# Kernel optimization log

Hardware: AMD Instinct MI355X
Metric: run time of the kernel (lower is better)

## Reference

```python
import jax, jax.numpy as jnp
import numpy as np

N_NODES = 100000
N_EDGES = 1600000
VOCAB = 1000
EMB_DIM = 64
OUT_DIM = 32


def setup_inputs() -> dict:
    key = jax.random.key(0)
    k1, k2, k3, k4, k5 = jax.random.split(key, 5)
    node_seq = jax.random.randint(k1, (N_NODES,), 0, VOCAB, dtype=jnp.int64)
    edge_index = jax.random.randint(k2, (2, N_EDGES), 0, N_NODES, dtype=jnp.int64)
    edge_weight = jax.random.uniform(k3, (N_EDGES,), dtype=jnp.float32)
    emb = jax.random.normal(k4, (VOCAB, EMB_DIM), dtype=jnp.float32)
    W = jax.random.normal(k5, (EMB_DIM, OUT_DIM), dtype=jnp.float32) * (1.0 / np.sqrt(EMB_DIM))
    b = jnp.zeros((OUT_DIM,), dtype=jnp.float32)
    return {"node_seq": node_seq, "edge_index": edge_index, "edge_weight": edge_weight,
            "emb": emb, "W": W, "b": b}


def reference(node_seq, edge_index, edge_weight, emb, W, b):
    N = node_seq.shape[0]
    # Embedding lookup: [N, EMB_DIM]
    x = emb[node_seq]
    # Linear transform first (GCNConv applies lin before propagate): [N, OUT_DIM]
    xw = x @ W
    # Add self loops with weight 1 (PyG GCNConv default add_self_loops=True, fill_value=1)
    loop = jnp.arange(N, dtype=edge_index.dtype)
    row = jnp.concatenate([edge_index[0], loop])
    col = jnp.concatenate([edge_index[1], loop])
    w = jnp.concatenate([edge_weight, jnp.ones((N,), dtype=edge_weight.dtype)])
    # Symmetric gcn_norm: deg over targets, norm = d^{-1/2}[row] * w * d^{-1/2}[col]
    deg = jax.ops.segment_sum(w, col, num_segments=N)
    dis = jnp.where(deg > 0, jax.lax.rsqrt(jnp.where(deg > 0, deg, 1.0)), 0.0)
    norm = dis[row] * w * dis[col]
    # Gather messages from source nodes, scale, scatter-add into targets
    msgs = norm[:, None] * xw[row]            # [E+N, OUT_DIM]
    out = jax.ops.segment_sum(msgs, col, num_segments=N) + b  # [N, OUT_DIM]
    # Mean pool over nodes
    return out.mean(axis=0)
```

## Files before the change

kernel.cpp:

```cpp
#include <hip/hip_runtime.h>

#define N_NODES 100000
#define N_EDGES 1600000
#define VOCAB   1000
#define EMB_DIM 64
#define OUT_DIM 32

#define BKT_BITS 9
#define BKT_SIZE 512
#define NBKT ((N_NODES + BKT_SIZE - 1) / BKT_SIZE)
#define CAP  12288
#define NSB  512
#define CHUNK (N_EDGES / NSB)

#define NBC 256
#define TBC 512

__device__ __forceinline__ void fatomic_add(float* p, float v) {
    unsafeAtomicAdd(p, v);
}

__global__ void k_init(int* __restrict__ cursors) {
    int i = blockIdx.x * blockDim.x + threadIdx.x;
    if (i < NBKT) cursors[i] = i * CAP;
}

__global__ void __launch_bounds__(256) k_scatter(
        const int* __restrict__ row, const int* __restrict__ col,
        const float* __restrict__ w, int* __restrict__ cursors,
        uint2* __restrict__ recs) {
    __shared__ uint2 stage[CHUNK];
    __shared__ unsigned char seg[CHUNK];
    __shared__ int cnt[NBKT], lofs[NBKT], gbase[NBKT];
    __shared__ int sc[256];
    const int tid = threadIdx.x;
    const int e0 = blockIdx.x * CHUNK;

    for (int i = tid; i < NBKT; i += 256) cnt[i] = 0;
    __syncthreads();
    for (int i = tid; i < CHUNK; i += 256)
        atomicAdd(&cnt[col[e0 + i] >> BKT_BITS], 1);
    __syncthreads();
    sc[tid] = (tid < NBKT) ? cnt[tid] : 0;
    __syncthreads();
    for (int d = 1; d < 256; d <<= 1) {
        int v = (tid >= d) ? sc[tid - d] : 0;
        __syncthreads();
        sc[tid] += v;
        __syncthreads();
    }
    if (tid < NBKT) {
        lofs[tid]  = sc[tid] - cnt[tid];
        gbase[tid] = atomicAdd(&cursors[tid], cnt[tid]);
        cnt[tid]   = 0;
    }
    __syncthreads();
    for (int i = tid; i < CHUNK; i += 256) {
        int c = col[e0 + i];
        int r = row[e0 + i];
        int b = c >> BKT_BITS;
        int p = lofs[b] + atomicAdd(&cnt[b], 1);
        stage[p] = make_uint2(((unsigned)r << BKT_BITS) | (unsigned)(c & (BKT_SIZE - 1)),
                              __float_as_uint(w[e0 + i]));
        seg[p] = (unsigned char)b;
    }
    __syncthreads();
    for (int i = tid; i < CHUNK; i += 256) {
        int b = seg[i];
        recs[gbase[b] + (i - lofs[b])] = stage[i];
    }
}

__global__ void __launch_bounds__(256) k_dis(
        const uint2* __restrict__ recs, const int* __restrict__ cursors,
        const int* __restrict__ node_seq, uint2* __restrict__ disseq) {
    __shared__ float acc[BKT_SIZE];
    const int b = blockIdx.x;
    for (int i = threadIdx.x; i < BKT_SIZE; i += 256) acc[i] = 0.0f;
    __syncthreads();
    const int base = b * CAP;
    const int cnt = cursors[b] - base;
    for (int i = threadIdx.x; i < cnt; i += 256) {
        uint2 r = recs[base + i];
        fatomic_add(&acc[r.x & (BKT_SIZE - 1)], __uint_as_float(r.y));
    }
    __syncthreads();
    const int n0 = b << BKT_BITS;
    for (int i = threadIdx.x; i < BKT_SIZE && n0 + i < N_NODES; i += 256)
        disseq[n0 + i] = make_uint2(__float_as_uint(__frsqrt_rn(1.0f + acc[i])),
                                    (unsigned)node_seq[n0 + i]);
}

__global__ void __launch_bounds__(512) k_coeff(
        const uint2* __restrict__ recs, const int* __restrict__ cursors,
        const uint2* __restrict__ disseq, float* __restrict__ gcoeff) {
    __shared__ float dloc[BKT_SIZE];
    __shared__ float lc[VOCAB];
    const int b = blockIdx.x;
    const int n0 = b << BKT_BITS;
    for (int i = threadIdx.x; i < VOCAB; i += 512) lc[i] = 0.0f;
    if (threadIdx.x < BKT_SIZE) {
        int n = n0 + threadIdx.x;
        dloc[threadIdx.x] = (n < N_NODES) ? __uint_as_float(disseq[n].x) : 0.0f;
    }
    __syncthreads();
    const int base = b * CAP;
    const int cnt = cursors[b] - base;
    for (int i = threadIdx.x; i < cnt; i += 512) {
        uint2 rec = recs[base + i];
        int lcol = rec.x & (BKT_SIZE - 1);
        int r    = rec.x >> BKT_BITS;
        uint2 ds = disseq[r];
        float norm = __uint_as_float(ds.x) * __uint_as_float(rec.y) * dloc[lcol];
        fatomic_add(&lc[ds.y], norm);
    }
    if (threadIdx.x < BKT_SIZE) {
        int n = n0 + threadIdx.x;
        if (n < N_NODES) {
            uint2 ds = disseq[n];
            float d = __uint_as_float(ds.x);
            fatomic_add(&lc[ds.y], d * d);
        }
    }
    __syncthreads();
    for (int i = threadIdx.x; i < VOCAB; i += 512)
        gcoeff[b * VOCAB + i] = lc[i];
}

__global__ void k_init_deg(float* __restrict__ deg) {
    int i = blockIdx.x * blockDim.x + threadIdx.x;
    if (i < N_NODES) deg[i] = 1.0f;
}
__global__ void k_deg(const int* __restrict__ col, const float* __restrict__ w,
                      float* __restrict__ deg) {
    int i = blockIdx.x * blockDim.x + threadIdx.x;
    if (i < N_EDGES) fatomic_add(&deg[col[i]], w[i]);
}
__global__ void k_dis_fb(float* __restrict__ deg) {
    int i = blockIdx.x * blockDim.x + threadIdx.x;
    if (i < N_NODES) deg[i] = __frsqrt_rn(deg[i]);
}
__global__ void __launch_bounds__(TBC) k_coeff_stream(
        const int* __restrict__ row, const int* __restrict__ col,
        const float* __restrict__ w, const float* __restrict__ dis,
        const int* __restrict__ node_seq, float* __restrict__ gcoeff) {
    __shared__ float lc[VOCAB];
    for (int i = threadIdx.x; i < VOCAB; i += TBC) lc[i] = 0.0f;
    __syncthreads();
    const int total = N_EDGES + N_NODES;
    const int stride = NBC * TBC;
    for (int i = blockIdx.x * TBC + threadIdx.x; i < total; i += stride) {
        if (i < N_EDGES) {
            int r = row[i];
            fatomic_add(&lc[node_seq[r]], dis[r] * w[i] * dis[col[i]]);
        } else {
            int n = i - N_EDGES;
            float d = dis[n];
            fatomic_add(&lc[node_seq[n]], d * d);
        }
    }
    __syncthreads();
    for (int i = threadIdx.x; i < VOCAB; i += TBC)
        gcoeff[blockIdx.x * VOCAB + i] = lc[i];
}

__global__ void __launch_bounds__(256) k_reduce(
        const float* __restrict__ gcoeff, float* __restrict__ coeff, int npart) {
    int g = blockIdx.x * 256 + threadIdx.x;
    int v = g >> 6;
    int l = g & 63;
    if (v >= VOCAB) return;
    float s = 0.0f;
    for (int p = l; p < npart; p += 64) s += gcoeff[p * VOCAB + v];
    for (int off = 32; off > 0; off >>= 1) s += __shfl_down(s, off, 64);
    if (l == 0) coeff[v] = s;
}

__global__ void __launch_bounds__(1024) k_final(
        const float* __restrict__ coeff, const float* __restrict__ emb,
        const float* __restrict__ W, const float* __restrict__ bias,
        float* __restrict__ out) {
    __shared__ float lc[VOCAB];
    __shared__ float tk[16 * 64];
    int t = threadIdx.x;
    for (int v = t; v < VOCAB; v += 1024) lc[v] = coeff[v];
    __syncthreads();

    int k = t & 63;
    int g = t >> 6;
    float p = 0.0f;
    for (int v = g; v < VOCAB; v += 16) p += lc[v] * emb[v * EMB_DIM + k];
    tk[g * 64 + k] = p;
    __syncthreads();

    if (t < 64) {
        float s = 0.0f;
        for (int gg = 0; gg < 16; ++gg) s += tk[gg * 64 + t];
        tk[t] = s;
    }
    __syncthreads();

    if (t < OUT_DIM) {
        float s = 0.0f;
        for (int kk = 0; kk < EMB_DIM; ++kk) s += tk[kk] * W[kk * OUT_DIM + t];
        out[t] = s * (1.0f / (float)N_NODES) + bias[t];
    }
}

extern "C" void kernel_launch(void* const* d_in, const int* in_sizes, int n_in,
                              void* d_out, int out_size, void* d_ws, size_t ws_size,
                              hipStream_t stream) {
    const int*   node_seq = (const int*)  d_in[0];
    const int*   eidx     = (const int*)  d_in[1];
    const float* ew       = (const float*)d_in[2];
    const float* emb      = (const float*)d_in[3];
    const float* W        = (const float*)d_in[4];
    const float* b        = (const float*)d_in[5];
    float*       out      = (float*)d_out;

    const int* row = eidx;
    const int* col = eidx + N_EDGES;

    char* wsb = (char*)d_ws;
    const size_t REC_BYTES = (size_t)NBKT * CAP * sizeof(uint2);
    const size_t need = REC_BYTES + 4096 + (size_t)N_NODES * 8
                      + (size_t)NBKT * VOCAB * 4 + VOCAB * 4 + 4096;

    if (ws_size >= need) {
        uint2* recs    = (uint2*)wsb;
        int*   cursors = (int*)(wsb + REC_BYTES);
        uint2* disseq  = (uint2*)(wsb + REC_BYTES + 4096);
        float* gcoeff  = (float*)(disseq + N_NODES);
        float* coeff   = gcoeff + (size_t)NBKT * VOCAB;

        k_init<<<1, 256, 0, stream>>>(cursors);
        k_scatter<<<NSB, 256, 0, stream>>>(row, col, ew, cursors, recs);
        k_dis<<<NBKT, 256, 0, stream>>>(recs, cursors, node_seq, disseq);
        k_coeff<<<NBKT, 512, 0, stream>>>(recs, cursors, disseq, gcoeff);
        k_reduce<<<(VOCAB * 64 + 255) / 256, 256, 0, stream>>>(gcoeff, coeff, NBKT);
        k_final<<<1, 1024, 0, stream>>>(coeff, emb, W, b, out);
    } else {
        float* dis    = (float*)wsb;
        float* gcoeff = dis + N_NODES;
        float* coeff  = gcoeff + (size_t)NBC * VOCAB;

        k_init_deg<<<(N_NODES + 255) / 256, 256, 0, stream>>>(dis);
        k_deg<<<(N_EDGES + 255) / 256, 256, 0, stream>>>(col, ew, dis);
        k_dis_fb<<<(N_NODES + 255) / 256, 256, 0, stream>>>(dis);
        k_coeff_stream<<<NBC, TBC, 0, stream>>>(row, col, ew, dis, node_seq, gcoeff);
        k_reduce<<<(VOCAB * 64 + 255) / 256, 256, 0, stream>>>(gcoeff, coeff, NBC);
        k_final<<<1, 1024, 0, stream>>>(coeff, emb, W, b, out);
    }
}
```

Before: 145.6 us.

## Fuse GCN pipeline into one cooperative kernel with grid syncs

Replaces the chain of six kernel launches with a single cooperative kernel that runs the phases (cursor init, bucket scatter, degree/dis, coefficient accumulation, reduction, final projection) separated by grid.sync(). The goal is to remove per-launch overhead and idle gaps between small kernels. The coefficient phase also splits each bucket across two blocks for more parallelism. The risks are grid-sync cost, lower occupancy from the large shared footprint (about 17KB plus other arrays at 512 threads), and the cooperative launch failing, which falls back to the old path. The fallback path also drops the workspace-size check and reduces gcoeff over NBKT partitions, while coeff is now placed after NPART partitions.

Result: slower. 423.0 us (+190.5%).

```diff
diff --git a/kernel.cpp b/kernel.cpp
--- a/kernel.cpp
+++ b/kernel.cpp
@@ -1,4 +1,7 @@
 #include <hip/hip_runtime.h>
+#include <hip/hip_cooperative_groups.h>
+
+namespace cg = cooperative_groups;
 
 #define N_NODES 100000
 #define N_EDGES 1600000
@@ -10,35 +13,193 @@
 #define BKT_SIZE 512
 #define NBKT ((N_NODES + BKT_SIZE - 1) / BKT_SIZE)
 #define CAP  12288
-#define NSB  512
-#define CHUNK (N_EDGES / NSB)
-
-#define NBC 256
-#define TBC 512
+#define GRID 512
+#define TPB  512
+#define CHUNK (N_EDGES / GRID)
+#define SPLIT 2
+#define NPART (NBKT * SPLIT)
 
 __device__ __forceinline__ void fatomic_add(float* p, float v) {
     unsafeAtomicAdd(p, v);
+}
+
+__global__ void __launch_bounds__(TPB, 4) k_fused(
+        const int* __restrict__ node_seq, const int* __restrict__ row,
+        const int* __restrict__ col, const float* __restrict__ ew,
+        const float* __restrict__ emb, const float* __restrict__ W,
+        const float* __restrict__ bias, float* __restrict__ out,
+        int* __restrict__ cursors, uint2* __restrict__ recs,
+        uint2* __restrict__ disseq, float* __restrict__ gcoeff,
+        float* __restrict__ coeff)
+{
+    cg::grid_group grid = cg::this_grid();
+    __shared__ uint2 stage[CHUNK];
+    __shared__ unsigned char seg[CHUNK];
+    __shared__ int cnt[NBKT], lofs[NBKT], gbase[NBKT];
+    __shared__ int sc[TPB];
+    __shared__ float acc[BKT_SIZE];
+    __shared__ float lc[VOCAB];
+    __shared__ float tk[8 * 64];
+
+    const int tid = threadIdx.x;
+    const int bid = blockIdx.x;
+
+    {
+        int g = bid * TPB + tid;
+        if (g < NBKT) cursors[g] = g * CAP;
+    }
+    grid.sync();
+
+    {
+        const int e0 = bid * CHUNK;
+        for (int i = tid; i < NBKT; i += TPB) cnt[i] = 0;
+        __syncthreads();
+        for (int i = tid; i < CHUNK; i += TPB)
+            atomicAdd(&cnt[col[e0 + i] >> BKT_BITS], 1);
+        __syncthreads();
+        sc[tid] = (tid < NBKT) ? cnt[tid] : 0;
+        __syncthreads();
+        for (int d = 1; d < TPB; d <<= 1) {
+            int v = (tid >= d) ? sc[tid - d] : 0;
+            __syncthreads();
+            sc[tid] += v;
+            __syncthreads();
+        }
+        if (tid < NBKT) {
+            lofs[tid]  = sc[tid] - cnt[tid];
+            gbase[tid] = atomicAdd(&cursors[tid], cnt[tid]);
+            cnt[tid]   = 0;
+        }
+        __syncthreads();
+        for (int i = tid; i < CHUNK; i += TPB) {
+            int c = col[e0 + i];
+            int r = row[e0 + i];
+            int b = c >> BKT_BITS;
+            int p = lofs[b] + atomicAdd(&cnt[b], 1);
+            stage[p] = make_uint2(((unsigned)r << BKT_BITS) | (unsigned)(c & (BKT_SIZE - 1)),
+                                  __float_as_uint(ew[e0 + i]));
+            seg[p] = (unsigned char)b;
+        }
+        __syncthreads();
+        for (int i = tid; i < CHUNK; i += TPB) {
+            int b = seg[i];
+            recs[gbase[b] + (i - lofs[b])] = stage[i];
+        }
+    }
+    grid.sync();
+
+    if (bid < NBKT) {
+        const int b = bid;
+        for (int i = tid; i < BKT_SIZE; i += TPB) acc[i] = 0.0f;
+        __syncthreads();
+        const int base = b * CAP;
+        const int c2 = cursors[b] - base;
+        for (int i = tid; i < c2; i += TPB) {
+            uint2 rr = recs[base + i];
+            fatomic_add(&acc[rr.x & (BKT_SIZE - 1)], __uint_as_float(rr.y));
+        }
+        __syncthreads();
+        const int n0 = b << BKT_BITS;
+        for (int i = tid; i < BKT_SIZE; i += TPB) {
+            int n = n0 + i;
+            if (n < N_NODES)
+                disseq[n] = make_uint2(__float_as_uint(__frsqrt_rn(1.0f + acc[i])),
+                                       (unsigned)node_seq[n]);
+        }
+    }
+    grid.sync();
+
+    if (bid < NPART) {
+        const int b = bid >> 1, half = bid & 1;
+        const int n0 = b << BKT_BITS;
+        for (int i = tid; i < VOCAB; i += TPB) lc[i] = 0.0f;
+        if (tid < BKT_SIZE) {
+            int n = n0 + tid;
+            acc[tid] = (n < N_NODES) ? __uint_as_float(disseq[n].x) : 0.0f;
+        }
+        __syncthreads();
+        const int base = b * CAP;
+        const int c3 = cursors[b] - base;
+        const int lo = half ? (c3 + 1) / 2 : 0;
+        const int hi = half ? c3 : (c3 + 1) / 2;
+        for (int i = lo + tid; i < hi; i += TPB) {
+            uint2 rec = recs[base + i];
+            int lcol = rec.x & (BKT_SIZE - 1);
+            int r    = rec.x >> BKT_BITS;
+            uint2 ds = disseq[r];
+            fatomic_add(&lc[ds.y],
+                __uint_as_float(ds.x) * __uint_as_float(rec.y) * acc[lcol]);
+        }
+        if (half == 0 && tid < BKT_SIZE) {
+            int n = n0 + tid;
+            if (n < N_NODES) {
+                uint2 ds = disseq[n];
+                float d = __uint_as_float(ds.x);
+                fatomic_add(&lc[ds.y], d * d);
+            }
+        }
+        __syncthreads();
+        for (int i = tid; i < VOCAB; i += TPB)
+            gcoeff[bid * VOCAB + i] = lc[i];
+    }
+    grid.sync();
+
+    {
+        int gw = (bid * TPB + tid) >> 6;
+        int l  = tid & 63;
+        if (gw < VOCAB) {
+            float s = 0.0f;
+            for (int p = l; p < NPART; p += 64) s += gcoeff[p * VOCAB + gw];
+            for (int off = 32; off > 0; off >>= 1) s += __shfl_down(s, off, 64);
+            if (l == 0) coeff[gw] = s;
+        }
+    }
+    grid.sync();
+
+    if (bid == 0) {
+        for (int v = tid; v < VOCAB; v += TPB) lc[v] = coeff[v];
+        __syncthreads();
+        int k = tid & 63;
+        int g = tid >> 6;
+        float p = 0.0f;
+        for (int v = g; v < VOCAB; v += 8) p += lc[v] * emb[v * EMB_DIM + k];
+        tk[g * 64 + k] = p;
+        __syncthreads();
+        if (tid < 64) {
+            float s = 0.0f;
+            for (int gg = 0; gg < 8; ++gg) s += tk[gg * 64 + tid];
+            tk[tid] = s;
+        }
+        __syncthreads();
+        if (tid < OUT_DIM) {
+            float s = 0.0f;
+            for (int kk = 0; kk < EMB_DIM; ++kk) s += tk[kk] * W[kk * OUT_DIM + tid];
+            out[tid] = s * (1.0f / (float)N_NODES) + bias[tid];
+        }
+    }
 }
 
 __global__ void k_init(int* __restrict__ cursors) {
     int i = blockIdx.x * blockDim.x + threadIdx.x;
     if (i < NBKT) cursors[i] = i * CAP;
 }
+
+#define NSB  512
+#define FCHUNK (N_EDGES / NSB)
 
 __global__ void __launch_bounds__(256) k_scatter(
         const int* __restrict__ row, const int* __restrict__ col,
         const float* __restrict__ w, int* __restrict__ cursors,
         uint2* __restrict__ recs) {
-    __shared__ uint2 stage[CHUNK];
-    __shared__ unsigned char seg[CHUNK];
+    __shared__ uint2 stage[FCHUNK];
+    __shared__ unsigned char seg[FCHUNK];
     __shared__ int cnt[NBKT], lofs[NBKT], gbase[NBKT];
     __shared__ int sc[256];
     const int tid = threadIdx.x;
-    const int e0 = blockIdx.x * CHUNK;
-
+    const int e0 = blockIdx.x * FCHUNK;
     for (int i = tid; i < NBKT; i += 256) cnt[i] = 0;
     __syncthreads();
-    for (int i = tid; i < CHUNK; i += 256)
+    for (int i = tid; i < FCHUNK; i += 256)
         atomicAdd(&cnt[col[e0 + i] >> BKT_BITS], 1);
     __syncthreads();
     sc[tid] = (tid < NBKT) ? cnt[tid] : 0;
@@ -55,7 +216,7 @@
         cnt[tid]   = 0;
     }
     __syncthreads();
-    for (int i = tid; i < CHUNK; i += 256) {
+    for (int i = tid; i < FCHUNK; i += 256) {
         int c = col[e0 + i];
         int r = row[e0 + i];
         int b = c >> BKT_BITS;
@@ -65,7 +226,7 @@
         seg[p] = (unsigned char)b;
     }
     __syncthreads();
-    for (int i = tid; i < CHUNK; i += 256) {
+    for (int i = tid; i < FCHUNK; i += 256) {
         int b = seg[i];
         recs[gbase[b] + (i - lofs[b])] = stage[i];
     }
@@ -111,8 +272,8 @@
         int lcol = rec.x & (BKT_SIZE - 1);
         int r    = rec.x >> BKT_BITS;
         uint2 ds = disseq[r];
-        float norm = __uint_as_float(ds.x) * __uint_as_float(rec.y) * dloc[lcol];
-        fatomic_add(&lc[ds.y], norm);
+        fatomic_add(&lc[ds.y],
+            __uint_as_float(ds.x) * __uint_as_float(rec.y) * dloc[lcol]);
     }
     if (threadIdx.x < BKT_SIZE) {
         int n = n0 + threadIdx.x;
@@ -125,43 +286,6 @@
     __syncthreads();
     for (int i = threadIdx.x; i < VOCAB; i += 512)
         gcoeff[b * VOCAB + i] = lc[i];
-}
-
-__global__ void k_init_deg(float* __restrict__ deg) {
-    int i = blockIdx.x * blockDim.x + threadIdx.x;
-    if (i < N_NODES) deg[i] = 1.0f;
-}
-__global__ void k_deg(const int* __restrict__ col, const float* __restrict__ w,
-                      float* __restrict__ deg) {
-    int i = blockIdx.x * blockDim.x + threadIdx.x;
-    if (i < N_EDGES) fatomic_add(&deg[col[i]], w[i]);
-}
-__global__ void k_dis_fb(float* __restrict__ deg) {
-    int i = blockIdx.x * blockDim.x + threadIdx.x;
-    if (i < N_NODES) deg[i] = __frsqrt_rn(deg[i]);
-}
-__global__ void __launch_bounds__(TBC) k_coeff_stream(
-        const int* __restrict__ row, const int* __restrict__ col,
-        const float* __restrict__ w, const float* __restrict__ dis,
-        const int* __restrict__ node_seq, float* __restrict__ gcoeff) {
-    __shared__ float lc[VOCAB];
-    for (int i = threadIdx.x; i < VOCAB; i += TBC) lc[i] = 0.0f;
-    __syncthreads();
-    const int total = N_EDGES + N_NODES;
-    const int stride = NBC * TBC;
-    for (int i = blockIdx.x * TBC + threadIdx.x; i < total; i += stride) {
-        if (i < N_EDGES) {
-            int r = row[i];
-            fatomic_add(&lc[node_seq[r]], dis[r] * w[i] * dis[col[i]]);
-        } else {
-            int n = i - N_EDGES;
-            float d = dis[n];
-            fatomic_add(&lc[node_seq[n]], d * d);
-        }
-    }
-    __syncthreads();
-    for (int i = threadIdx.x; i < VOCAB; i += TBC)
-        gcoeff[blockIdx.x * VOCAB + i] = lc[i];
 }
 
 __global__ void __launch_bounds__(256) k_reduce(
@@ -185,21 +309,18 @@
     int t = threadIdx.x;
     for (int v = t; v < VOCAB; v += 1024) lc[v] = coeff[v];
     __syncthreads();
-
     int k = t & 63;
     int g = t >> 6;
     float p = 0.0f;
     for (int v = g; v < VOCAB; v += 16) p += lc[v] * emb[v * EMB_DIM + k];
     tk[g * 64 + k] = p;
     __syncthreads();
-
     if (t < 64) {
         float s = 0.0f;
         for (int gg = 0; gg < 16; ++gg) s += tk[gg * 64 + t];
         tk[t] = s;
     }
     __syncthreads();
-
     if (t < OUT_DIM) {
         float s = 0.0f;
         for (int kk = 0; kk < EMB_DIM; ++kk) s += tk[kk] * W[kk * OUT_DIM + t];
@@ -215,7 +336,7 @@
     const float* ew       = (const float*)d_in[2];
     const float* emb      = (const float*)d_in[3];
     const float* W        = (const float*)d_in[4];
-    const float* b        = (const float*)d_in[5];
+    const float* bias     = (const float*)d_in[5];
     float*       out      = (float*)d_out;
 
     const int* row = eidx;
@@ -223,32 +344,25 @@
 
     char* wsb = (char*)d_ws;
     const size_t REC_BYTES = (size_t)NBKT * CAP * sizeof(uint2);
-    const size_t need = REC_BYTES + 4096 + (size_t)N_NODES * 8
-                      + (size_t)NBKT * VOCAB * 4 + VOCAB * 4 + 4096;
-
-    if (ws_size >= need) {
-        uint2* recs    = (uint2*)wsb;
-        int*   cursors = (int*)(wsb + REC_BYTES);
-        uint2* disseq  = (uint2*)(wsb + REC_BYTES + 4096);
-        float* gcoeff  = (float*)(disseq + N_NODES);
-        float* coeff   = gcoeff + (size_t)NBKT * VOCAB;
-
+    uint2* recs    = (uint2*)wsb;
+    int*   cursors = (int*)(wsb + REC_BYTES);
+    uint2* disseq  = (uint2*)(wsb + REC_BYTES + 4096);
+    float* gcoeff  = (float*)(disseq + N_NODES);
+    float* coeff   = gcoeff + (size_t)NPART * VOCAB;
+
+    void* args[] = {(void*)&node_seq, (void*)&row, (void*)&col, (void*)&ew,
+                    (void*)&emb, (void*)&W, (void*)&bias, (void*)&out,
+                    (void*)&cursors, (void*)&recs, (void*)&disseq,
+                    (void*)&gcoeff, (void*)&coeff};
+    hipError_t err = hipLaunchCooperativeKernel((const void*)k_fused,
+                                                dim3(GRID), dim3(TPB),
+                                                args, 0, stream);
+    if (err != hipSuccess) {
         k_init<<<1, 256, 0, stream>>>(cursors);
         k_scatter<<<NSB, 256, 0, stream>>>(row, col, ew, cursors, recs);
         k_dis<<<NBKT, 256, 0, stream>>>(recs, cursors, node_seq, disseq);
         k_coeff<<<NBKT, 512, 0, stream>>>(recs, cursors, disseq, gcoeff);
         k_reduce<<<(VOCAB * 64 + 255) / 256, 256, 0, stream>>>(gcoeff, coeff, NBKT);
-        k_final<<<1, 1024, 0, stream>>>(coeff, emb, W, b, out);
-    } else {
-        float* dis    = (float*)wsb;
-        float* gcoeff = dis + N_NODES;
-        float* coeff  = gcoeff + (size_t)NBC * VOCAB;
-
-        k_init_deg<<<(N_NODES + 255) / 256, 256, 0, stream>>>(dis);
-        k_deg<<<(N_EDGES + 255) / 256, 256, 0, stream>>>(col, ew, dis);
-        k_dis_fb<<<(N_NODES + 255) / 256, 256, 0, stream>>>(dis);
-        k_coeff_stream<<<NBC, TBC, 0, stream>>>(row, col, ew, dis, node_seq, gcoeff);
-        k_reduce<<<(VOCAB * 64 + 255) / 256, 256, 0, stream>>>(gcoeff, coeff, NBC);
-        k_final<<<1, 1024, 0, stream>>>(coeff, emb, W, b, out);
-    }
-}
+        k_final<<<1, 1024, 0, stream>>>(coeff, emb, W, bias, out);
+    }
+}
```

## Split coefficient work per bucket, fuse reduce and final, retune scatter chunking

Applied to the files above, without the earlier changes.

The coefficient pass now uses four blocks per destination bucket instead of one, which raises parallelism. The separate reduce and final kernels are merged into one kernel that accumulates the embedding projection atomically, and a last-block-done counter finishes the output. Scatter chunks shrink (1000 blocks instead of 512) and bucket capacity is cut. Cursors become relative offsets, and the workspace fallback path is removed. The risks are atomic contention on the 64-wide accumulation vector and overflowing a bucket's capacity on skewed inputs.

Result: slower. 167.8 us (+15.3%).

```diff
diff --git a/kernel.cpp b/kernel.cpp
--- a/kernel.cpp
+++ b/kernel.cpp
@@ -9,20 +9,23 @@
 #define BKT_BITS 9
 #define BKT_SIZE 512
 #define NBKT ((N_NODES + BKT_SIZE - 1) / BKT_SIZE)
-#define CAP  12288
-#define NSB  512
+#define CAP  10240
+#define NSB  1000
 #define CHUNK (N_EDGES / NSB)
-
-#define NBC 256
-#define TBC 512
+#define SPLIT 4
+#define NPART (NBKT * SPLIT)
+#define NRF_BLOCKS 250
 
 __device__ __forceinline__ void fatomic_add(float* p, float v) {
     unsafeAtomicAdd(p, v);
 }
 
-__global__ void k_init(int* __restrict__ cursors) {
-    int i = blockIdx.x * blockDim.x + threadIdx.x;
-    if (i < NBKT) cursors[i] = i * CAP;
+__global__ void k_init(int* __restrict__ cursors, int* __restrict__ done,
+                       float* __restrict__ tvec) {
+    int i = threadIdx.x;
+    if (i < NBKT) cursors[i] = 0;
+    if (i == 0) *done = 0;
+    if (i < 64) tvec[i] = 0.0f;
 }
 
 __global__ void __launch_bounds__(256) k_scatter(
@@ -30,7 +33,7 @@
         const float* __restrict__ w, int* __restrict__ cursors,
         uint2* __restrict__ recs) {
     __shared__ uint2 stage[CHUNK];
-    __shared__ unsigned char seg[CHUNK];
+    __shared__ unsigned short seg[CHUNK];
     __shared__ int cnt[NBKT], lofs[NBKT], gbase[NBKT];
     __shared__ int sc[256];
     const int tid = threadIdx.x;
@@ -51,7 +54,7 @@
     }
     if (tid < NBKT) {
         lofs[tid]  = sc[tid] - cnt[tid];
-        gbase[tid] = atomicAdd(&cursors[tid], cnt[tid]);
+        gbase[tid] = tid * CAP + atomicAdd(&cursors[tid], cnt[tid]);
         cnt[tid]   = 0;
     }
     __syncthreads();
@@ -62,7 +65,7 @@
         int p = lofs[b] + atomicAdd(&cnt[b], 1);
         stage[p] = make_uint2(((unsigned)r << BKT_BITS) | (unsigned)(c & (BKT_SIZE - 1)),
                               __float_as_uint(w[e0 + i]));
-        seg[p] = (unsigned char)b;
+        seg[p] = (unsigned short)b;
     }
     __syncthreads();
     for (int i = tid; i < CHUNK; i += 256) {
@@ -71,24 +74,27 @@
     }
 }
 
-__global__ void __launch_bounds__(256) k_dis(
+__global__ void __launch_bounds__(512) k_dis(
         const uint2* __restrict__ recs, const int* __restrict__ cursors,
         const int* __restrict__ node_seq, uint2* __restrict__ disseq) {
     __shared__ float acc[BKT_SIZE];
     const int b = blockIdx.x;
-    for (int i = threadIdx.x; i < BKT_SIZE; i += 256) acc[i] = 0.0f;
+    if (threadIdx.x < BKT_SIZE) acc[threadIdx.x] = 0.0f;
     __syncthreads();
     const int base = b * CAP;
-    const int cnt = cursors[b] - base;
-    for (int i = threadIdx.x; i < cnt; i += 256) {
+    const int cnt = cursors[b];
+    for (int i = threadIdx.x; i < cnt; i += 512) {
         uint2 r = recs[base + i];
         fatomic_add(&acc[r.x & (BKT_SIZE - 1)], __uint_as_float(r.y));
     }
     __syncthreads();
     const int n0 = b << BKT_BITS;
-    for (int i = threadIdx.x; i < BKT_SIZE && n0 + i < N_NODES; i += 256)
-        disseq[n0 + i] = make_uint2(__float_as_uint(__frsqrt_rn(1.0f + acc[i])),
-                                    (unsigned)node_seq[n0 + i]);
+    if (threadIdx.x < BKT_SIZE) {
+        int n = n0 + threadIdx.x;
+        if (n < N_NODES)
+            disseq[n] = make_uint2(__float_as_uint(__frsqrt_rn(1.0f + acc[threadIdx.x])),
+                                   (unsigned)node_seq[n]);
+    }
 }
 
 __global__ void __launch_bounds__(512) k_coeff(
@@ -96,7 +102,7 @@
         const uint2* __restrict__ disseq, float* __restrict__ gcoeff) {
     __shared__ float dloc[BKT_SIZE];
     __shared__ float lc[VOCAB];
-    const int b = blockIdx.x;
+    const int b = blockIdx.x >> 2, s = blockIdx.x & 3;
     const int n0 = b << BKT_BITS;
     for (int i = threadIdx.x; i < VOCAB; i += 512) lc[i] = 0.0f;
     if (threadIdx.x < BKT_SIZE) {
@@ -105,16 +111,18 @@
     }
     __syncthreads();
     const int base = b * CAP;
-    const int cnt = cursors[b] - base;
-    for (int i = threadIdx.x; i < cnt; i += 512) {
+    const int cnt = cursors[b];
+    const int lo = (cnt * s) >> 2;
+    const int hi = (cnt * (s + 1)) >> 2;
+    for (int i = lo + threadIdx.x; i < hi; i += 512) {
         uint2 rec = recs[base + i];
         int lcol = rec.x & (BKT_SIZE - 1);
         int r    = rec.x >> BKT_BITS;
         uint2 ds = disseq[r];
-        float norm = __uint_as_float(ds.x) * __uint_as_float(rec.y) * dloc[lcol];
-        fatomic_add(&lc[ds.y], norm);
-    }
-    if (threadIdx.x < BKT_SIZE) {
+        fatomic_add(&lc[ds.y],
+            __uint_as_float(ds.x) * __uint_as_float(rec.y) * dloc[lcol]);
+    }
+    if (s == 0 && threadIdx.x < BKT_SIZE) {
         int n = n0 + threadIdx.x;
         if (n < N_NODES) {
             uint2 ds = disseq[n];
@@ -124,86 +132,43 @@
     }
     __syncthreads();
     for (int i = threadIdx.x; i < VOCAB; i += 512)
-        gcoeff[b * VOCAB + i] = lc[i];
-}
-
-__global__ void k_init_deg(float* __restrict__ deg) {
-    int i = blockIdx.x * blockDim.x + threadIdx.x;
-    if (i < N_NODES) deg[i] = 1.0f;
-}
-__global__ void k_deg(const int* __restrict__ col, const float* __restrict__ w,
-                      float* __restrict__ deg) {
-    int i = blockIdx.x * blockDim.x + threadIdx.x;
-    if (i < N_EDGES) fatomic_add(&deg[col[i]], w[i]);
-}
-__global__ void k_dis_fb(float* __restrict__ deg) {
-    int i = blockIdx.x * blockDim.x + threadIdx.x;
-    if (i < N_NODES) deg[i] = __frsqrt_rn(deg[i]);
-}
-__global__ void __launch_bounds__(TBC) k_coeff_stream(
-        const int* __restrict__ row, const int* __restrict__ col,
-        const float* __restrict__ w, const float* __restrict__ dis,
-        const int* __restrict__ node_seq, float* __restrict__ gcoeff) {
-    __shared__ float lc[VOCAB];
-    for (int i = threadIdx.x; i < VOCAB; i += TBC) lc[i] = 0.0f;
-    __syncthreads();
-    const int total = N_EDGES + N_NODES;
-    const int stride = NBC * TBC;
-    for (int i = blockIdx.x * TBC + threadIdx.x; i < total; i += stride) {
-        if (i < N_EDGES) {
-            int r = row[i];
-            fatomic_add(&lc[node_seq[r]], dis[r] * w[i] * dis[col[i]]);
-        } else {
-            int n = i - N_EDGES;
-            float d = dis[n];
-            fatomic_add(&lc[node_seq[n]], d * d);
+        gcoeff[blockIdx.x * VOCAB + i] = lc[i];
+}
+
+__global__ void __launch_bounds__(256) k_reduce_final(
+        const float* __restrict__ gcoeff, const float* __restrict__ emb,
+        const float* __restrict__ W, const float* __restrict__ bias,
+        float* __restrict__ tvec, int* __restrict__ done,
+        float* __restrict__ out) {
+    __shared__ int lastflag;
+    const int tid = threadIdx.x;
+    const int v = (blockIdx.x * 256 + tid) >> 6;
+    const int l = tid & 63;
+    if (v < VOCAB) {
+        float s = 0.0f;
+        for (int p = l; p < NPART; p += 64) s += gcoeff[p * VOCAB + v];
+        for (int off = 32; off > 0; off >>= 1) s += __shfl_down(s, off, 64);
+        float cv = __shfl(s, 0, 64);
+        fatomic_add(&tvec[l], cv * emb[v * EMB_DIM + l]);
+    }
+    __syncthreads();
+    if (tid == 0) {
+        __threadfence();
+        int t = atomicAdd(done, 1);
+        lastflag = (t == NRF_BLOCKS - 1) ? 1 : 0;
+    }
+    __syncthreads();
+    if (lastflag) {
+        __threadfence();
+        __shared__ float tk[EMB_DIM];
+        if (tid < EMB_DIM) tk[tid] = ((volatile float*)tvec)[tid];
+        __syncthreads();
+        if (tid < OUT_DIM) {
+            float s = 0.0f;
+            #pragma unroll
+            for (int k = 0; k < EMB_DIM; ++k) s += tk[k] * W[k * OUT_DIM + tid];
+            out[tid] = s * (1.0f / (float)N_NODES) + bias[tid];
         }
-    }
-    __syncthreads();
-    for (int i = threadIdx.x; i < VOCAB; i += TBC)
-        gcoeff[blockIdx.x * VOCAB + i] = lc[i];
-}
-
-__global__ void __launch_bounds__(256) k_reduce(
-        const float* __restrict__ gcoeff, float* __restrict__ coeff, int npart) {
-    int g = blockIdx.x * 256 + threadIdx.x;
-    int v = g >> 6;
-    int l = g & 63;
-    if (v >= VOCAB) return;
-    float s = 0.0f;
-    for (int p = l; p < npart; p += 64) s += gcoeff[p * VOCAB + v];
-    for (int off = 32; off > 0; off >>= 1) s += __shfl_down(s, off, 64);
-    if (l == 0) coeff[v] = s;
-}
-
-__global__ void __launch_bounds__(1024) k_final(
-        const float* __restrict__ coeff, const float* __restrict__ emb,
-        const float* __restrict__ W, const float* __restrict__ bias,
-        float* __restrict__ out) {
-    __shared__ float lc[VOCAB];
-    __shared__ float tk[16 * 64];
-    int t = threadIdx.x;
-    for (int v = t; v < VOCAB; v += 1024) lc[v] = coeff[v];
-    __syncthreads();
-
-    int k = t & 63;
-    int g = t >> 6;
-    float p = 0.0f;
-    for (int v = g; v < VOCAB; v += 16) p += lc[v] * emb[v * EMB_DIM + k];
-    tk[g * 64 + k] = p;
-    __syncthreads();
-
-    if (t < 64) {
-        float s = 0.0f;
-        for (int gg = 0; gg < 16; ++gg) s += tk[gg * 64 + t];
-        tk[t] = s;
-    }
-    __syncthreads();
-
-    if (t < OUT_DIM) {
-        float s = 0.0f;
-        for (int kk = 0; kk < EMB_DIM; ++kk) s += tk[kk] * W[kk * OUT_DIM + t];
-        out[t] = s * (1.0f / (float)N_NODES) + bias[t];
     }
 }
 
@@ -215,7 +180,7 @@
     const float* ew       = (const float*)d_in[2];
     const float* emb      = (const float*)d_in[3];
     const float* W        = (const float*)d_in[4];
-    const float* b        = (const float*)d_in[5];
+    const float* bias     = (const float*)d_in[5];
     float*       out      = (float*)d_out;
 
     const int* row = eidx;
@@ -223,32 +188,17 @@
 
     char* wsb = (char*)d_ws;
     const size_t REC_BYTES = (size_t)NBKT * CAP * sizeof(uint2);
-    const size_t need = REC_BYTES + 4096 + (size_t)N_NODES * 8
-                      + (size_t)NBKT * VOCAB * 4 + VOCAB * 4 + 4096;
-
-    if (ws_size >= need) {
-        uint2* recs    = (uint2*)wsb;
-        int*   cursors = (int*)(wsb + REC_BYTES);
-        uint2* disseq  = (uint2*)(wsb + REC_BYTES + 4096);
-        float* gcoeff  = (float*)(disseq + N_NODES);
-        float* coeff   = gcoeff + (size_t)NBKT * VOCAB;
-
-        k_init<<<1, 256, 0, stream>>>(cursors);
-        k_scatter<<<NSB, 256, 0, stream>>>(row, col, ew, cursors, recs);
-        k_dis<<<NBKT, 256, 0, stream>>>(recs, cursors, node_seq, disseq);
-        k_coeff<<<NBKT, 512, 0, stream>>>(recs, cursors, disseq, gcoeff);
-        k_reduce<<<(VOCAB * 64 + 255) / 256, 256, 0, stream>>>(gcoeff, coeff, NBKT);
-        k_final<<<1, 1024, 0, stream>>>(coeff, emb, W, b, out);
-    } else {
-        float* dis    = (float*)wsb;
-        float* gcoeff = dis + N_NODES;
-        float* coeff  = gcoeff + (size_t)NBC * VOCAB;
-
-        k_init_deg<<<(N_NODES + 255) / 256, 256, 0, stream>>>(dis);
-        k_deg<<<(N_EDGES + 255) / 256, 256, 0, stream>>>(col, ew, dis);
-        k_dis_fb<<<(N_NODES + 255) / 256, 256, 0, stream>>>(dis);
-        k_coeff_stream<<<NBC, TBC, 0, stream>>>(row, col, ew, dis, node_seq, gcoeff);
-        k_reduce<<<(VOCAB * 64 + 255) / 256, 256, 0, stream>>>(gcoeff, coeff, NBC);
-        k_final<<<1, 1024, 0, stream>>>(coeff, emb, W, b, out);
-    }
-}
+    uint2* recs    = (uint2*)wsb;
+    int*   cursors = (int*)(wsb + REC_BYTES);
+    int*   done    = cursors + NBKT;
+    float* tvec    = (float*)(done + 1);
+    uint2* disseq  = (uint2*)(wsb + REC_BYTES + 4096);
+    float* gcoeff  = (float*)(disseq + N_NODES);
+
+    k_init<<<1, 512, 0, stream>>>(cursors, done, tvec);
+    k_scatter<<<NSB, 256, 0, stream>>>(row, col, ew, cursors, recs);
+    k_dis<<<NBKT, 512, 0, stream>>>(recs, cursors, node_seq, disseq);
+    k_coeff<<<NPART, 512, 0, stream>>>(recs, cursors, disseq, gcoeff);
+    k_reduce_final<<<NRF_BLOCKS, 256, 0, stream>>>(gcoeff, emb, W, bias,
+                                                   tvec, done, out);
+}
```
